# Performance work log

Hardware: AMD Instinct MI355X
Metric: run time of the kernel (lower is better)

Reference implementation:

```python
import jax, jax.numpy as jnp
from jax import lax
import numpy as np

B, N, D = 64, 512, 2


def _dtw_cost(x, y):
    """Exact DTW with L1 point distance. x: (n, d), y: (m, d).
    Returns terminal cumulative cost D[n-1, m-1], which equals the sum of
    ||x_i - y_j||_1 over the optimal warping path (what the torch module
    accumulates after fastdtw path search)."""
    # pairwise L1 cost matrix (n, m)
    C = jnp.sum(jnp.abs(x[:, None, :] - y[None, :, :]), axis=-1)
    row0 = jnp.cumsum(C[0])  # D[0, :]
    big = jnp.asarray(jnp.inf, C.dtype)

    def row_step(prev, c):
        # prev = D[i-1, :]; c = C[i, :]
        diag = jnp.concatenate([jnp.full((1,), big), prev[:-1]])  # D[i-1, j-1]

        def col_step(left, inp):
            ci, up, dg = inp
            cur = ci + jnp.minimum(jnp.minimum(up, dg), left)
            return cur, cur

        _, cur = lax.scan(col_step, big, (c, prev, diag))
        return cur, None

    final_row, _ = lax.scan(row_step, row0, C[1:])
    return final_row[-1]


def setup_inputs() -> dict:
    key = jax.random.key(0)
    k1, k2 = jax.random.split(key)
    pred = jax.random.normal(k1, (B, N, D), dtype=jnp.float32)
    target = jax.random.normal(k2, (B, N, D), dtype=jnp.float32)
    return {"pred": pred, "target": target}


def reference(pred, target):
    # mean over batch of per-sequence DTW path L1 loss
    per_batch = jax.vmap(_dtw_cost)(pred, target)  # (B,)
    return jnp.mean(per_batch)
```

## Files before the change

kernel.cpp:

```cpp
#include <hip/hip_runtime.h>
#include <math.h>


typedef float f32x2 __attribute__((ext_vector_type(2)));

constexpr int NSEQ  = 512;
constexpr int BATCH = 64;
constexpr int P     = 8;
constexpr int LANES = 64;
constexpr int FRONT = 64;
constexpr int XSN   = FRONT + 581;

__device__ __forceinline__ float dpp_wshr1_inf(float v) {
    int r = __builtin_amdgcn_update_dpp(0x7F800000, __float_as_int(v),
                                        0x138, 0xF, 0xF, false);
    return __int_as_float(r);
}

__global__ __launch_bounds__(LANES) void dtw_fused(
    const float* __restrict__ pred,
    const float* __restrict__ target,
    float* __restrict__ out,
    float* __restrict__ ws)
{
    const int b = blockIdx.x;
    const int j = threadIdx.x;

    __shared__ f32x2 xs[XSN];

    #pragma unroll
    for (int t = 0; t < NSEQ / LANES; ++t) {
        const int idx = t * LANES + j;
        xs[FRONT + idx] = reinterpret_cast<const f32x2*>(pred)[b * NSEQ + idx];
    }
    f32x2 nY[P];
    #pragma unroll
    for (int c = 0; c < P; ++c) {
        const f32x2 y = reinterpret_cast<const f32x2*>(target)[b * NSEQ + j * P + c];
        nY[c].x = -y.x; nY[c].y = -y.y;
    }
    __syncthreads();

    const float INF = __builtin_inff();
    float prev[P];
    #pragma unroll
    for (int c = 0; c < P; ++c) prev[c] = INF;
    float dg0 = INF;

    if (j == 0) {
        const f32x2 x = xs[FRONT];
        f32x2 d0 = x + nY[0];
        float v = fabsf(d0.x) + fabsf(d0.y);
        prev[0] = v;
        #pragma unroll
        for (int c = 1; c < P; ++c) {
            f32x2 dc = x + nY[c];
            v += fabsf(dc.x) + fabsf(dc.y);
            prev[c] = v;
        }
    }

    auto step = [&](float left, f32x2 x, int kk, bool guard) {
        float v_[P];
        {
            f32x2 d = x + nY[0];
            v_[0] = fabsf(d.x) + fabsf(d.y) + fminf(fminf(prev[0], dg0), left);
        }
        float pm1 = prev[0];
        #pragma unroll
        for (int c = 1; c < P; ++c) {
            f32x2 d = x + nY[c];
            const float pc = prev[c];
            v_[c] = fabsf(d.x) + fabsf(d.y) + fminf(fminf(pc, pm1), v_[c - 1]);
            pm1 = pc;
        }
        if (guard) {
            const bool act = (unsigned)(kk - j) < (unsigned)NSEQ;
            #pragma unroll
            for (int c = 0; c < P; ++c) prev[c] = act ? v_[c] : prev[c];
        } else {
            #pragma unroll
            for (int c = 0; c < P; ++c) prev[c] = v_[c];
        }
        dg0 = left;
    };

    f32x2 r0, r1, r2, r3;
    {
        const int base = FRONT + 1 - j;
        r0 = xs[base]; r1 = xs[base + 1]; r2 = xs[base + 2]; r3 = xs[base + 3];
    }

    auto block4 = [&](int k4, bool guard) {
        const int base = FRONT + k4 + 4 - j;
        const f32x2 n0 = xs[base],     n1 = xs[base + 1];
        const f32x2 n2 = xs[base + 2], n3 = xs[base + 3];
        float left;
        left = dpp_wshr1_inf(prev[P - 1]); step(left, r0, k4 + 0, guard);
        left = dpp_wshr1_inf(prev[P - 1]); step(left, r1, k4 + 1, guard);
        left = dpp_wshr1_inf(prev[P - 1]); step(left, r2, k4 + 2, guard);
        left = dpp_wshr1_inf(prev[P - 1]); step(left, r3, k4 + 3, guard);
        r0 = n0; r1 = n1; r2 = n2; r3 = n3;
    };

    #pragma unroll 1
    for (int k4 = 1; k4 <= 61; k4 += 4)   block4(k4, true);
    #pragma unroll 1
    for (int k4 = 65; k4 <= 505; k4 += 4) block4(k4, false);
    #pragma unroll 1
    for (int k4 = 509; k4 <= 573; k4 += 4) block4(k4, true);

    float* per_batch = ws;
    unsigned* flag = reinterpret_cast<unsigned*>(ws + BATCH);
    if (j == LANES - 1) per_batch[b] = prev[P - 1];
    __threadfence();
    unsigned old = 0;
    if (j == 0) old = atomicAdd(flag, 1u);
    old = __shfl(old, 0);
    if (old == BATCH - 1) {
        __threadfence();
        float v = per_batch[j];
        #pragma unroll
        for (int off = 32; off >= 1; off >>= 1) v += __shfl_down(v, off);
        if (j == 0) out[0] = v * (1.0f / BATCH);
    }
}

extern "C" void kernel_launch(void* const* d_in, const int* in_sizes, int n_in,
                              void* d_out, int out_size, void* d_ws, size_t ws_size,
                              hipStream_t stream) {
    const float* pred   = (const float*)d_in[0];
    const float* target = (const float*)d_in[1];
    float* out = (float*)d_out;
    float* ws  = (float*)d_ws;

    hipMemsetAsync((char*)d_ws + BATCH * sizeof(float), 0, sizeof(unsigned), stream);
    dtw_fused<<<BATCH, LANES, 0, stream>>>(pred, target, out, ws);
}
```

Measured before the change: 58.23 us.

## Split DTW columns into two 4-wide halves processed as staggered wavefronts

Each lane now owns two groups of 4 columns, one in the first 256 and one in the second 256 columns, instead of 8 contiguous columns. The second half runs 64 steps behind the first and takes its left boundary from lane 63 of the first half through a DPP rotate. This shortens the serial dependency chain per anti-diagonal step from 8 to 4 and gives two independent chains per step for instruction-level parallelism. In exchange the wavefront needs 638 steps instead of 576, the x loads are doubled, and there is an extra drain loop.

```diff
diff --git a/kernel.cpp b/kernel.cpp
--- a/kernel.cpp
+++ b/kernel.cpp
@@ -6,14 +6,18 @@
 
 constexpr int NSEQ  = 512;
 constexpr int BATCH = 64;
-constexpr int P     = 8;
 constexpr int LANES = 64;
-constexpr int FRONT = 64;
-constexpr int XSN   = FRONT + 581;
+constexpr int FRONT = 128;
+constexpr int XSN   = 768;
 
-__device__ __forceinline__ float dpp_wshr1_inf(float v) {
-    int r = __builtin_amdgcn_update_dpp(0x7F800000, __float_as_int(v),
+__device__ __forceinline__ float dpp_shr1(float v, float old) {
+    int r = __builtin_amdgcn_update_dpp(__float_as_int(old), __float_as_int(v),
                                         0x138, 0xF, 0xF, false);
+    return __int_as_float(r);
+}
+__device__ __forceinline__ float dpp_ror1(float v) {
+    int r = __builtin_amdgcn_update_dpp(0, __float_as_int(v),
+                                        0x13C, 0xF, 0xF, false);
     return __int_as_float(r);
 }
 
@@ -33,86 +37,106 @@
         const int idx = t * LANES + j;
         xs[FRONT + idx] = reinterpret_cast<const f32x2*>(pred)[b * NSEQ + idx];
     }
-    f32x2 nY[P];
+    f32x2 nYA[4], nYB[4];
     #pragma unroll
-    for (int c = 0; c < P; ++c) {
-        const f32x2 y = reinterpret_cast<const f32x2*>(target)[b * NSEQ + j * P + c];
-        nY[c].x = -y.x; nY[c].y = -y.y;
+    for (int c = 0; c < 4; ++c) {
+        const f32x2 ya = reinterpret_cast<const f32x2*>(target)[b * NSEQ + 4*j + c];
+        nYA[c].x = -ya.x; nYA[c].y = -ya.y;
+        const f32x2 yb = reinterpret_cast<const f32x2*>(target)[b * NSEQ + 256 + 4*j + c];
+        nYB[c].x = -yb.x; nYB[c].y = -yb.y;
     }
     __syncthreads();
 
     const float INF = __builtin_inff();
-    float prev[P];
+    float pA[4], pB[4];
     #pragma unroll
-    for (int c = 0; c < P; ++c) prev[c] = INF;
-    float dg0 = INF;
+    for (int c = 0; c < 4; ++c) { pA[c] = INF; pB[c] = INF; }
+    float dgA = INF, dgB = INF;
 
     if (j == 0) {
         const f32x2 x = xs[FRONT];
-        f32x2 d0 = x + nY[0];
-        float v = fabsf(d0.x) + fabsf(d0.y);
-        prev[0] = v;
+        float v = 0.f;
         #pragma unroll
-        for (int c = 1; c < P; ++c) {
-            f32x2 dc = x + nY[c];
-            v += fabsf(dc.x) + fabsf(dc.y);
-            prev[c] = v;
+        for (int c = 0; c < 4; ++c) {
+            const f32x2 d = x + nYA[c];
+            v += fabsf(d.x) + fabsf(d.y);
+            pA[c] = v;
         }
     }
 
-    auto step = [&](float left, f32x2 x, int kk, bool guard) {
-        float v_[P];
-        {
-            f32x2 d = x + nY[0];
-            v_[0] = fabsf(d.x) + fabsf(d.y) + fminf(fminf(prev[0], dg0), left);
+    f32x2 xA = xs[FRONT + 1 - j];
+    f32x2 xB = xs[FRONT + 1 - j - 64];
+
+    auto step = [&](int k, bool gA, bool gB) {
+        const float leftA = dpp_shr1(pA[3], INF);
+        const float rA    = dpp_ror1(pA[3]);
+        const float leftB = dpp_shr1(pB[3], rA);
+        const f32x2 xAn = xs[FRONT + k + 1 - j];
+        const f32x2 xBn = xs[FRONT + k + 1 - j - 64];
+        float vA[4], vB[4];
+        { const f32x2 d = xA + nYA[0];
+          vA[0] = fabsf(d.x) + fabsf(d.y) + fminf(fminf(pA[0], dgA), leftA); }
+        { const f32x2 d = xB + nYB[0];
+          vB[0] = fabsf(d.x) + fabsf(d.y) + fminf(fminf(pB[0], dgB), leftB); }
+        float pmA = pA[0], pmB = pB[0];
+        #pragma unroll
+        for (int c = 1; c < 4; ++c) {
+            { const f32x2 d = xA + nYA[c];
+              vA[c] = fabsf(d.x) + fabsf(d.y) + fminf(fminf(pA[c], pmA), vA[c-1]);
+              pmA = pA[c]; }
+            { const f32x2 d = xB + nYB[c];
+              vB[c] = fabsf(d.x) + fabsf(d.y) + fminf(fminf(pB[c], pmB), vB[c-1]);
+              pmB = pB[c]; }
         }
-        float pm1 = prev[0];
-        #pragma unroll
-        for (int c = 1; c < P; ++c) {
-            f32x2 d = x + nY[c];
-            const float pc = prev[c];
-            v_[c] = fabsf(d.x) + fabsf(d.y) + fminf(fminf(pc, pm1), v_[c - 1]);
-            pm1 = pc;
-        }
-        if (guard) {
-            const bool act = (unsigned)(kk - j) < (unsigned)NSEQ;
+        if (gA) {
+            const bool a = (unsigned)(k - j) < (unsigned)NSEQ;
             #pragma unroll
-            for (int c = 0; c < P; ++c) prev[c] = act ? v_[c] : prev[c];
+            for (int c = 0; c < 4; ++c) pA[c] = a ? vA[c] : pA[c];
         } else {
             #pragma unroll
-            for (int c = 0; c < P; ++c) prev[c] = v_[c];
+            for (int c = 0; c < 4; ++c) pA[c] = vA[c];
         }
-        dg0 = left;
-    };
-
-    f32x2 r0, r1, r2, r3;
-    {
-        const int base = FRONT + 1 - j;
-        r0 = xs[base]; r1 = xs[base + 1]; r2 = xs[base + 2]; r3 = xs[base + 3];
-    }
-
-    auto block4 = [&](int k4, bool guard) {
-        const int base = FRONT + k4 + 4 - j;
-        const f32x2 n0 = xs[base],     n1 = xs[base + 1];
-        const f32x2 n2 = xs[base + 2], n3 = xs[base + 3];
-        float left;
-        left = dpp_wshr1_inf(prev[P - 1]); step(left, r0, k4 + 0, guard);
-        left = dpp_wshr1_inf(prev[P - 1]); step(left, r1, k4 + 1, guard);
-        left = dpp_wshr1_inf(prev[P - 1]); step(left, r2, k4 + 2, guard);
-        left = dpp_wshr1_inf(prev[P - 1]); step(left, r3, k4 + 3, guard);
-        r0 = n0; r1 = n1; r2 = n2; r3 = n3;
+        if (gB) {
+            const bool a = (unsigned)(k - j - 64) < (unsigned)NSEQ;
+            #pragma unroll
+            for (int c = 0; c < 4; ++c) pB[c] = a ? vB[c] : pB[c];
+        } else {
+            #pragma unroll
+            for (int c = 0; c < 4; ++c) pB[c] = vB[c];
+        }
+        dgA = leftA; dgB = leftB;
+        xA = xAn; xB = xBn;
     };
 
     #pragma unroll 1
-    for (int k4 = 1; k4 <= 61; k4 += 4)   block4(k4, true);
+    for (int k = 1; k < 128; ++k)   step(k, true, true);
+    #pragma unroll 2
+    for (int k = 128; k < 512; ++k) step(k, false, false);
+    #pragma unroll 2
+    for (int k = 512; k < 576; ++k) step(k, true, false);
     #pragma unroll 1
-    for (int k4 = 65; k4 <= 505; k4 += 4) block4(k4, false);
-    #pragma unroll 1
-    for (int k4 = 509; k4 <= 573; k4 += 4) block4(k4, true);
+    for (int k = 576; k < 639; ++k) {
+        const float leftB = dpp_shr1(pB[3], INF);
+        const f32x2 xBn = xs[FRONT + k + 1 - j - 64];
+        float vB[4];
+        { const f32x2 d = xB + nYB[0];
+          vB[0] = fabsf(d.x) + fabsf(d.y) + fminf(fminf(pB[0], dgB), leftB); }
+        float pmB = pB[0];
+        #pragma unroll
+        for (int c = 1; c < 4; ++c) {
+            const f32x2 d = xB + nYB[c];
+            vB[c] = fabsf(d.x) + fabsf(d.y) + fminf(fminf(pB[c], pmB), vB[c-1]);
+            pmB = pB[c];
+        }
+        const bool a = (unsigned)(k - j - 64) < (unsigned)NSEQ;
+        #pragma unroll
+        for (int c = 0; c < 4; ++c) pB[c] = a ? vB[c] : pB[c];
+        dgB = leftB; xB = xBn;
+    }
 
     float* per_batch = ws;
     unsigned* flag = reinterpret_cast<unsigned*>(ws + BATCH);
-    if (j == LANES - 1) per_batch[b] = prev[P - 1];
+    if (j == LANES - 1) per_batch[b] = pB[3];
     __threadfence();
     unsigned old = 0;
     if (j == 0) old = atomicAdd(flag, 1u);
```

New measurement: 74.53 us. 1.28x slower.

## Process two DTW rows per wavefront step with zero-padded prologue and packed adds

Applied to the files above, without the earlier changes.

Restructures the wavefront so each lane advances two x rows per macro step, loading pairs of points as float4 from LDS and exchanging two shifted values by DPP per step. The active-lane guards are dropped: the x buffer is zero-padded at both ends and an initial boundary computation seeds the state instead. The subtractions use inline v_pk_add_f32. This halves the number of sequential dependency rounds and cross-lane shuffles and removes the guard selects, in exchange for a more complex dependency chain per step and higher register pressure. Correctness depends on the padding values producing harmless results outside the valid range.

```diff
diff --git a/kernel.cpp b/kernel.cpp
--- a/kernel.cpp
+++ b/kernel.cpp
@@ -3,18 +3,24 @@
 
 
 typedef float f32x2 __attribute__((ext_vector_type(2)));
+typedef float f32x4 __attribute__((ext_vector_type(4)));
 
 constexpr int NSEQ  = 512;
 constexpr int BATCH = 64;
+constexpr int LANES = 64;
 constexpr int P     = 8;
-constexpr int LANES = 64;
-constexpr int FRONT = 64;
-constexpr int XSN   = FRONT + 581;
+constexpr int FRONT = 63;
+constexpr int XS4N  = 384;
 
-__device__ __forceinline__ float dpp_wshr1_inf(float v) {
+__device__ __forceinline__ float dpp_shr1_inf(float v) {
     int r = __builtin_amdgcn_update_dpp(0x7F800000, __float_as_int(v),
                                         0x138, 0xF, 0xF, false);
     return __int_as_float(r);
+}
+__device__ __forceinline__ f32x2 pk_add(f32x2 a, f32x2 b) {
+    f32x2 d;
+    asm("v_pk_add_f32 %0, %1, %2" : "=v"(d) : "v"(a), "v"(b));
+    return d;
 }
 
 __global__ __launch_bounds__(LANES) void dtw_fused(
@@ -26,13 +32,16 @@
     const int b = blockIdx.x;
     const int j = threadIdx.x;
 
-    __shared__ f32x2 xs[XSN];
+    __shared__ f32x4 xs4[XS4N];
 
+    const f32x4* pred4 = reinterpret_cast<const f32x4*>(pred) + b * (NSEQ / 2);
     #pragma unroll
-    for (int t = 0; t < NSEQ / LANES; ++t) {
-        const int idx = t * LANES + j;
-        xs[FRONT + idx] = reinterpret_cast<const f32x2*>(pred)[b * NSEQ + idx];
-    }
+    for (int t = 0; t < 4; ++t)
+        xs4[FRONT + t * LANES + j] = pred4[t * LANES + j];
+    if (j < FRONT) xs4[j] = f32x4{0.f, 0.f, 0.f, 0.f};
+    xs4[FRONT + 256 + j] = f32x4{0.f, 0.f, 0.f, 0.f};
+    if (j == 0) xs4[383] = f32x4{0.f, 0.f, 0.f, 0.f};
+
     f32x2 nY[P];
     #pragma unroll
     for (int c = 0; c < P; ++c) {
@@ -42,77 +51,67 @@
     __syncthreads();
 
     const float INF = __builtin_inff();
-    float prev[P];
-    #pragma unroll
-    for (int c = 0; c < P; ++c) prev[c] = INF;
-    float dg0 = INF;
+    float p[P], q[P], aA[P], aB[P];
+    float dg = INF;
 
-    if (j == 0) {
-        const f32x2 x = xs[FRONT];
-        f32x2 d0 = x + nY[0];
-        float v = fabsf(d0.x) + fabsf(d0.y);
-        prev[0] = v;
+    f32x4 x0 = xs4[FRONT - j];
+    f32x4 xc1 = xs4[FRONT + 1 - j];
+    f32x4 xc2 = xs4[FRONT + 2 - j];
+    {
+        const f32x2 xa = {x0.x, x0.y}, xb = {x0.z, x0.w};
+        const float lA0 = (j == 0) ? 0.0f : INF;
+        { const f32x2 d = pk_add(xa, nY[0]); aA[0] = fabsf(d.x) + fabsf(d.y) + lA0; }
         #pragma unroll
         for (int c = 1; c < P; ++c) {
-            f32x2 dc = x + nY[c];
-            v += fabsf(dc.x) + fabsf(dc.y);
-            prev[c] = v;
+            const f32x2 d = pk_add(xa, nY[c]);
+            aA[c] = fabsf(d.x) + fabsf(d.y) + aA[c - 1];
+        }
+        { const f32x2 d = pk_add(xb, nY[0]); p[0] = fabsf(d.x) + fabsf(d.y) + aA[0]; }
+        #pragma unroll
+        for (int c = 1; c < P; ++c) {
+            const f32x2 d = pk_add(xb, nY[c]);
+            p[c] = fabsf(d.x) + fabsf(d.y)
+                 + fminf(fminf(aA[c], aA[c - 1]), p[c - 1]);
         }
     }
 
-    auto step = [&](float left, f32x2 x, int kk, bool guard) {
-        float v_[P];
-        {
-            f32x2 d = x + nY[0];
-            v_[0] = fabsf(d.x) + fabsf(d.y) + fminf(fminf(prev[0], dg0), left);
-        }
-        float pm1 = prev[0];
+    auto macro = [&](const float (&pb)[P], float (&ob)[P],
+                     const float (&ain)[P], float (&aout)[P], f32x4 x4) {
+        const float lA = dpp_shr1_inf(ain[P - 1]);
+        const float lB = dpp_shr1_inf(pb[P - 1]);
+        const f32x2 xa = {x4.x, x4.y}, xb = {x4.z, x4.w};
+        { const f32x2 d = pk_add(xa, nY[0]);
+          aout[0] = fabsf(d.x) + fabsf(d.y) + fminf(fminf(pb[0], dg), lA); }
         #pragma unroll
         for (int c = 1; c < P; ++c) {
-            f32x2 d = x + nY[c];
-            const float pc = prev[c];
-            v_[c] = fabsf(d.x) + fabsf(d.y) + fminf(fminf(pc, pm1), v_[c - 1]);
-            pm1 = pc;
+            const f32x2 d = pk_add(xa, nY[c]);
+            aout[c] = fabsf(d.x) + fabsf(d.y)
+                    + fminf(fminf(pb[c], pb[c - 1]), aout[c - 1]);
         }
-        if (guard) {
-            const bool act = (unsigned)(kk - j) < (unsigned)NSEQ;
-            #pragma unroll
-            for (int c = 0; c < P; ++c) prev[c] = act ? v_[c] : prev[c];
-        } else {
-            #pragma unroll
-            for (int c = 0; c < P; ++c) prev[c] = v_[c];
+        { const f32x2 d = pk_add(xb, nY[0]);
+          ob[0] = fabsf(d.x) + fabsf(d.y) + fminf(fminf(aout[0], lA), lB); }
+        #pragma unroll
+        for (int c = 1; c < P; ++c) {
+            const f32x2 d = pk_add(xb, nY[c]);
+            ob[c] = fabsf(d.x) + fabsf(d.y)
+                  + fminf(fminf(aout[c], aout[c - 1]), ob[c - 1]);
         }
-        dg0 = left;
+        dg = lB;
     };
 
-    f32x2 r0, r1, r2, r3;
-    {
-        const int base = FRONT + 1 - j;
-        r0 = xs[base]; r1 = xs[base + 1]; r2 = xs[base + 2]; r3 = xs[base + 3];
+    #pragma unroll 2
+    for (int mm = 0; mm < 159; ++mm) {
+        const int m1 = 1 + 2 * mm;
+        const f32x4 xn1 = xs4[FRONT + m1 + 2 - j];
+        const f32x4 xn2 = xs4[FRONT + m1 + 3 - j];
+        macro(p, q, aA, aB, xc1);
+        macro(q, p, aB, aA, xc2);
+        xc1 = xn1; xc2 = xn2;
     }
-
-    auto block4 = [&](int k4, bool guard) {
-        const int base = FRONT + k4 + 4 - j;
-        const f32x2 n0 = xs[base],     n1 = xs[base + 1];
-        const f32x2 n2 = xs[base + 2], n3 = xs[base + 3];
-        float left;
-        left = dpp_wshr1_inf(prev[P - 1]); step(left, r0, k4 + 0, guard);
-        left = dpp_wshr1_inf(prev[P - 1]); step(left, r1, k4 + 1, guard);
-        left = dpp_wshr1_inf(prev[P - 1]); step(left, r2, k4 + 2, guard);
-        left = dpp_wshr1_inf(prev[P - 1]); step(left, r3, k4 + 3, guard);
-        r0 = n0; r1 = n1; r2 = n2; r3 = n3;
-    };
-
-    #pragma unroll 1
-    for (int k4 = 1; k4 <= 61; k4 += 4)   block4(k4, true);
-    #pragma unroll 1
-    for (int k4 = 65; k4 <= 505; k4 += 4) block4(k4, false);
-    #pragma unroll 1
-    for (int k4 = 509; k4 <= 573; k4 += 4) block4(k4, true);
 
     float* per_batch = ws;
     unsigned* flag = reinterpret_cast<unsigned*>(ws + BATCH);
-    if (j == LANES - 1) per_batch[b] = prev[P - 1];
+    if (j == LANES - 1) per_batch[b] = p[P - 1];
     __threadfence();
     unsigned old = 0;
     if (j == 0) old = atomicAdd(flag, 1u);
```

Result: slower. 60.67 us (+4.2%).
